# Kernel tuning notes

Hardware: AMD Instinct MI355X
Metric: run time of the kernel (lower is better)

The kernel has to match this reference:

```python
import jax, jax.numpy as jnp
import numpy as np

B, L, E, H, D, DFF = 2, 2048, 1024, 16, 64, 4096
SCALE = D ** 0.5


def rmsnorm(x):
    # NOTE: original uses mean(x*x)**0.5 with no eps and no learned scale
    rms = jnp.sqrt(jnp.mean(x * x, axis=-1, keepdims=True))
    return x / rms


def alibi_matrix():
    i = jnp.arange(L)
    dists = -jnp.abs(i[None, :] - i[:, None]).astype(jnp.float32)  # [L, L]
    slopes = 2.0 ** (-jnp.linspace(1.0, 8.0, H))                   # [H]
    alibi = slopes[:, None, None] * dists                          # [H, L, L]
    causal = jnp.tril(jnp.ones((L, L), dtype=bool))
    return jnp.where(causal[None], alibi, -jnp.inf)[None]          # [1, H, L, L]


def setup_inputs() -> dict:
    key = jax.random.key(0)
    ks = jax.random.split(key, 16)
    s = 0.02
    return {
        "X": jax.random.normal(ks[0], (B, L, E), jnp.float32),
        "encoder_out": jax.random.normal(ks[1], (B, L, E), jnp.float32),
        # self-attention params
        "Wqkv": jax.random.normal(ks[2], (E, 3 * H * D), jnp.float32) * s,
        "bqkv": jnp.zeros((3 * H * D,), jnp.float32),
        "Wo_sa": jax.random.normal(ks[3], (H * D, E), jnp.float32) * s,
        "bo_sa": jnp.zeros((E,), jnp.float32),
        # cross-attention params (computed by torch module but its forward returns X, so unused)
        "Wq": jax.random.normal(ks[4], (E, H * D), jnp.float32) * s,
        "bq": jnp.zeros((H * D,), jnp.float32),
        "Wkv": jax.random.normal(ks[5], (E, 2 * H * D), jnp.float32) * s,
        "bkv": jnp.zeros((2 * H * D,), jnp.float32),
        "Wo_ca": jax.random.normal(ks[6], (H * D, E), jnp.float32) * s,
        "bo_ca": jnp.zeros((E,), jnp.float32),
        # GLU FFN params (bias=False)
        "Ww": jax.random.normal(ks[7], (E, DFF), jnp.float32) * s,
        "Wv": jax.random.normal(ks[8], (E, DFF), jnp.float32) * s,
        "Wout": jax.random.normal(ks[9], (DFF, E), jnp.float32) * s,
    }


def reference(X, encoder_out, Wqkv, bqkv, Wo_sa, bo_sa, Wq, bq, Wkv, bkv,
              Wo_ca, bo_ca, Ww, Wv, Wout):
    alibi = alibi_matrix()

    # ---- self-attention (pre-norm + residual) ----
    h = rmsnorm(X)
    qkv = (h @ Wqkv + bqkv).reshape(B, L, H, 3, D)
    Q, K, V = qkv[..., 0, :], qkv[..., 1, :], qkv[..., 2, :]      # [B, L, H, D]
    scores = jnp.einsum('blhd,bmhd->bhlm', Q, K) / SCALE + alibi  # [B, H, L, L]
    attn = jax.nn.softmax(scores, axis=-1)
    ctx = jnp.einsum('bhlm,bmhd->blhd', attn, V).reshape(B, L, H * D)
    X = X + ctx @ Wo_sa + bo_sa

    # ---- cross-attention stage ----
    # Faithful to source: CrossAttention.forward returns its input X (the
    # normalized tensor) rather than the attention output, so this block is
    # X + rmsnorm(X). Cross-attn params never affect the output.
    X = X + rmsnorm(X)

    # ---- GLU FFN (pre-norm + residual), exact (erf) GELU as in torch F.gelu ----
    h = rmsnorm(X)
    ff = jax.nn.gelu(h @ Ww, approximate=False) * (h @ Wv)
    X = X + ff @ Wout
    return X
```

## Files before the change

### kernel.cpp

```cpp
#include <hip/hip_runtime.h>

#define B_SZ 2
#define L_SEQ 2048
#define E_DIM 1024
#define NH 16
#define DH 64
#define DFF_DIM 4096
#define ROWS (B_SZ * L_SEQ)
#define NCID 80

typedef __attribute__((ext_vector_type(8))) short short8;
typedef __attribute__((ext_vector_type(4))) float f32x4;

__device__ __forceinline__ short f2bf(float f) {
  unsigned u = __builtin_bit_cast(unsigned, f);
  u = (u + 0x7FFFu + ((u >> 16) & 1u)) >> 16;
  return (short)u;
}
__device__ __forceinline__ float bf2f(short s) {
  unsigned u = ((unsigned)(unsigned short)s) << 16;
  return __builtin_bit_cast(float, u);
}

__device__ __forceinline__ void async_copy16(const void* g, void* l) {
  __builtin_amdgcn_global_load_lds(
      (const __attribute__((address_space(1))) void*)g,
      (__attribute__((address_space(3))) void*)l, 16, 0, 0);
}

__device__ __forceinline__ float block_sum256(float v) {
  __shared__ float sbuf[4];
#pragma unroll
  for (int off = 32; off > 0; off >>= 1) v += __shfl_xor(v, off, 64);
  int lane = threadIdx.x & 63, w = threadIdx.x >> 6;
  if (lane == 0) sbuf[w] = v;
  __syncthreads();
  return sbuf[0] + sbuf[1] + sbuf[2] + sbuf[3];
}

__global__ __launch_bounds__(256) void prep_all(
    const float* __restrict__ Wqkv, const float* __restrict__ Wo,
    const float* __restrict__ Ww, const float* __restrict__ Wv,
    const float* __restrict__ Wout, const float* __restrict__ X,
    short* __restrict__ WqkT, short* __restrict__ Wv3T,
    short* __restrict__ WoT, short* __restrict__ Bcat,
    short* __restrict__ WoutT, short* __restrict__ H) {
  __shared__ float tile[32][33];
  int b = blockIdx.x;
  if (b < 16384) {
    const float* W;
    int K, N, mode, bx, by;
    short* Wt;
    if (b < 3072) {
      W = Wqkv; Wt = nullptr; K = 1024; N = 3072; mode = 0;
      bx = b % 96; by = b / 96;
    } else if (b < 4096) {
      int c = b - 3072;
      W = Wo; Wt = WoT; K = 1024; N = 1024; mode = 1;
      bx = c & 31; by = c >> 5;
    } else if (b < 8192) {
      int c = b - 4096;
      W = Ww; Wt = Bcat; K = 1024; N = 4096; mode = 2;
      bx = c & 127; by = c >> 7;
    } else if (b < 12288) {
      int c = b - 8192;
      W = Wv; Wt = Bcat; K = 1024; N = 4096; mode = 3;
      bx = c & 127; by = c >> 7;
    } else {
      int c = b - 12288;
      W = Wout; Wt = WoutT; K = 4096; N = 1024; mode = 1;
      bx = c & 31; by = c >> 5;
    }
    int n0 = bx * 32, k0 = by * 32;
    int tx = threadIdx.x & 31, ty = threadIdx.x >> 5;
#pragma unroll
    for (int i = 0; i < 4; i++)
      tile[ty + 8 * i][tx] = W[(size_t)(k0 + ty + 8 * i) * N + n0 + tx];
    __syncthreads();
#pragma unroll
    for (int i = 0; i < 4; i++) {
      int n = n0 + ty + 8 * i;
      short val = f2bf(tile[tx][ty + 8 * i]);
      if (mode == 0) {
        int h = n / 192, rem = n - h * 192;
        if (rem < 128)
          WqkT[(size_t)(h * 128 + rem) * 1024 + k0 + tx] = val;
        else
          Wv3T[(size_t)(h * 64 + rem - 128) * 1024 + k0 + tx] = val;
      } else {
        int orow = (mode == 1) ? n
                               : ((n >> 6) * 128 + (n & 63) + (mode == 3 ? 64 : 0));
        Wt[(size_t)orow * K + k0 + tx] = val;
      }
    }
  } else {
    size_t row = b - 16384;
    float4 v = ((const float4*)(X + row * E_DIM))[threadIdx.x];
    float ss = v.x * v.x + v.y * v.y + v.z * v.z + v.w * v.w;
    ss = block_sum256(ss);
    float inv = rsqrtf(ss * (1.0f / E_DIM));
    short* h = H + row * E_DIM + (size_t)threadIdx.x * 4;
    h[0] = f2bf(v.x * inv);
    h[1] = f2bf(v.y * inv);
    h[2] = f2bf(v.z * inv);
    h[3] = f2bf(v.w * inv);
  }
}

__global__ __launch_bounds__(256) void resid_rms_fused(
    const float* __restrict__ X, const float* __restrict__ P0,
    const float* __restrict__ P1, const float* __restrict__ bias,
    float* __restrict__ Xout, short* __restrict__ H) {
  size_t row = blockIdx.x;
  int t = threadIdx.x;
  float4 v = ((const float4*)(X + row * E_DIM))[t];
  float4 a = ((const float4*)(P0 + row * E_DIM))[t];
  float4 b = ((const float4*)(P1 + row * E_DIM))[t];
  float4 c = ((const float4*)bias)[t];
  v.x += a.x + b.x + c.x;
  v.y += a.y + b.y + c.y;
  v.z += a.z + b.z + c.z;
  v.w += a.w + b.w + c.w;
  float ss = v.x * v.x + v.y * v.y + v.z * v.z + v.w * v.w;
  ss = block_sum256(ss);
  float inv = rsqrtf(ss * (1.0f / E_DIM));
  float4 o;
  o.x = v.x * (1.0f + inv);
  o.y = v.y * (1.0f + inv);
  o.z = v.z * (1.0f + inv);
  o.w = v.w * (1.0f + inv);
  ((float4*)(Xout + row * E_DIM))[t] = o;
  short* h = H + row * E_DIM + (size_t)t * 4;
  h[0] = f2bf(v.x * inv);
  h[1] = f2bf(v.y * inv);
  h[2] = f2bf(v.z * inv);
  h[3] = f2bf(v.w * inv);
}

__global__ __launch_bounds__(256, 2) void gemm_bt(
    const short* __restrict__ A, const short* __restrict__ Bt,
    const float* __restrict__ bias, void* __restrict__ out,
    void* __restrict__ out2, int M, int N, int K, int epi, int ksplit) {
  __shared__ short smem[128 * 32 * 4];
  short* As0 = smem;
  short* Bs0 = smem + 4096;
  short* As1 = smem + 8192;
  short* Bs1 = smem + 12288;
  int t = threadIdx.x;
  int lane = t & 63;
  int quad = lane >> 4, l16 = lane & 15;
  int wave = t >> 6;
  int wr = wave >> 1, wc = wave & 1;
  int m0 = blockIdx.y * 128, n0 = blockIdx.x * 128;
  int klen = K / ksplit;
  int kstart = blockIdx.z * klen;

  f32x4 acc[4][4];
#pragma unroll
  for (int i = 0; i < 4; i++)
#pragma unroll
    for (int j = 0; j < 4; j++) acc[i][j] = (f32x4){0.f, 0.f, 0.f, 0.f};

  for (int k0 = kstart; k0 < kstart + klen; k0 += 64) {
    __syncthreads();
#pragma unroll
    for (int p = 0; p < 2; p++) {
      int s = p * 256 + t;
      int mm = s >> 2, kk = (s & 3) * 8;
      const short* ag = A + (size_t)(m0 + mm) * K + k0 + kk;
      const short* bg = Bt + (size_t)(n0 + mm) * K + k0 + kk;
      async_copy16(ag, As0 + (size_t)s * 8);
      async_copy16(bg, Bs0 + (size_t)s * 8);
      async_copy16(ag + 32, As1 + (size_t)s * 8);
      async_copy16(bg + 32, Bs1 + (size_t)s * 8);
    }
    __syncthreads();
#pragma unroll
    for (int half = 0; half < 2; half++) {
      const short* As = half ? As1 : As0;
      const short* Bs = half ? Bs1 : Bs0;
      short8 af[4], bfv[4];
#pragma unroll
      for (int i = 0; i < 4; i++) {
        af[i] = *(const short8*)&As[(wr * 64 + i * 16 + l16) * 32 + quad * 8];
        bfv[i] = *(const short8*)&Bs[(wc * 64 + i * 16 + l16) * 32 + quad * 8];
      }
#pragma unroll
      for (int mi = 0; mi < 4; mi++)
#pragma unroll
        for (int ni = 0; ni < 4; ni++)
          acc[mi][ni] = __builtin_amdgcn_mfma_f32_16x16x32_bf16(
              af[mi], bfv[ni], acc[mi][ni], 0, 0, 0);
    }
  }

  if (epi == 5) {
    __syncthreads();
    short* xbuf = smem;
    if (wc == 0) {
#pragma unroll
      for (int mi = 0; mi < 4; mi++)
#pragma unroll
        for (int ni = 0; ni < 4; ni++)
#pragma unroll
          for (int r = 0; r < 4; r++) {
            int rowl = wr * 64 + mi * 16 + quad * 4 + r;
            float v = acc[mi][ni][r];
            float g = 0.5f * v * (1.0f + erff(v * 0.70710678118654752f));
            xbuf[rowl * 68 + ni * 16 + l16] = f2bf(g);
          }
    }
    __syncthreads();
    if (wc == 1) {
      short* FF = (short*)out;
#pragma unroll
      for (int mi = 0; mi < 4; mi++)
#pragma unroll
        for (int ni = 0; ni < 4; ni++)
#pragma unroll
          for (int r = 0; r < 4; r++) {
            int rowl = wr * 64 + mi * 16 + quad * 4 + r;
            int coll = ni * 16 + l16;
            float w = bf2f(xbuf[rowl * 68 + coll]);
            FF[(size_t)(m0 + rowl) * DFF_DIM + blockIdx.x * 64 + coll] =
                f2bf(w * acc[mi][ni][r]);
          }
    }
    return;
  }

#pragma unroll
  for (int mi = 0; mi < 4; mi++) {
#pragma unroll
    for (int ni = 0; ni < 4; ni++) {
      int col = n0 + wc * 64 + ni * 16 + l16;
#pragma unroll
      for (int r = 0; r < 4; r++) {
        int row = m0 + wr * 64 + mi * 16 + quad * 4 + r;
        float v = acc[mi][ni][r];
        if (epi == 4) {
          float* po = (float*)out + (size_t)blockIdx.z * ((size_t)M * N);
          po[(size_t)row * N + col] = v;
        } else if (epi == 6) {
          v += bias[(col >> 7) * 192 + (col & 127)];
          int h = col >> 7, d = col & 63;
          short* dst = ((col >> 6) & 1) ? (short*)out2 : (short*)out;
          int bb = row >> 11, l = row & 2047;
          dst[((size_t)(bb * NH + h) * L_SEQ + l) * DH + d] = f2bf(v);
        } else if (epi == 7) {
          v += bias[(row >> 6) * 192 + 128 + (row & 63)];
          int bb = col >> 11, l = col & 2047;
          ((short*)out)[((size_t)(bb * NH + (row >> 6)) * DH + (row & 63)) *
                            L_SEQ +
                        l] = f2bf(v);
        } else {
          unsafeAtomicAdd((float*)out + (size_t)row * N + col, v);
        }
      }
    }
  }
}

__global__ __launch_bounds__(256) void attn_k(const short* __restrict__ Qh,
                                              const short* __restrict__ Kh,
                                              const short* __restrict__ VTh,
                                              float* __restrict__ OP,
                                              float* __restrict__ RS) {
  int cid = blockIdx.x;
  int bh = blockIdx.y;
  int b = bh >> 4, h = bh & 15;
  int qt, ch;
  if (cid < 8) {
    qt = cid; ch = 0;
  } else if (cid < 24) {
    qt = 8 + ((cid - 8) >> 1); ch = (cid - 8) & 1;
  } else if (cid < 48) {
    qt = 16 + (cid - 24) / 3; ch = (cid - 24) % 3;
  } else {
    qt = 24 + ((cid - 48) >> 2); ch = (cid - 48) & 3;
  }
  int t0 = ch * 8;
  int tend = min(t0 + 8, qt + 1);

  int t = threadIdx.x;
  int wave = t >> 6, lane = t & 63;
  int quad = lane >> 4, l16 = lane & 15;

  __shared__ short kt[64 * 72];
  __shared__ short vt[64 * 72];
  __shared__ short pb[4 * 16 * 70];

  const float slope = exp2f(-(1.0f + (7.0f / 15.0f) * (float)h));
  int iw = qt * 64 + wave * 16;

  short8 qf[2];
  {
    const short* qp = Qh + ((size_t)bh * L_SEQ + iw + l16) * DH + quad * 8;
    qf[0] = *(const short8*)(qp);
    qf[1] = *(const short8*)(qp + 32);
  }

  f32x4 o[4];
#pragma unroll
  for (int i = 0; i < 4; i++) o[i] = (f32x4){0.f, 0.f, 0.f, 0.f};
  float rs[4] = {0.f, 0.f, 0.f, 0.f};
  float crow[4];
  int irow[4];
#pragma unroll
  for (int r = 0; r < 4; r++) {
    irow[r] = iw + quad * 4 + r;
    crow[r] = -slope * (float)irow[r] - 8.0f;
  }

  int sr = t >> 3, sc = (t & 7) * 8;
  const short* kg = Kh + (size_t)bh * L_SEQ * DH;
  const short* vg = VTh + (size_t)bh * DH * L_SEQ;
  short8 kreg[2], vreg[2];
  auto loadKV = [&](int j0) {
    kreg[0] = *(const short8*)(kg + (size_t)(j0 + sr) * DH + sc);
    kreg[1] = *(const short8*)(kg + (size_t)(j0 + sr + 32) * DH + sc);
    vreg[0] = *(const short8*)(vg + (size_t)sr * L_SEQ + j0 + sc);
    vreg[1] = *(const short8*)(vg + (size_t)(sr + 32) * L_SEQ + j0 + sc);
  };
  loadKV(t0 * 64);

  short* pw = &pb[wave * 16 * 70];
  for (int tix = t0; tix < tend; ++tix) {
    int j0 = tix * 64;
    __syncthreads();
    *(short8*)&kt[sr * 72 + sc] = kreg[0];
    *(short8*)&kt[(sr + 32) * 72 + sc] = kreg[1];
    *(short8*)&vt[sr * 72 + sc] = vreg[0];
    *(short8*)&vt[(sr + 32) * 72 + sc] = vreg[1];
    __syncthreads();
    if (tix + 1 < tend) loadKV(j0 + 64);

    f32x4 s[4];
#pragma unroll
    for (int nt = 0; nt < 4; nt++) {
      f32x4 a = (f32x4){0.f, 0.f, 0.f, 0.f};
#pragma unroll
      for (int ks = 0; ks < 2; ks++) {
        short8 bf =
            *(const short8*)&kt[(nt * 16 + l16) * 72 + ks * 32 + quad * 8];
        a = __builtin_amdgcn_mfma_f32_16x16x32_bf16(qf[ks], bf, a, 0, 0, 0);
      }
      s[nt] = a;
    }
    bool diag = (tix == qt);
#pragma unroll
    for (int nt = 0; nt < 4; nt++) {
      int j = j0 + nt * 16 + l16;
      float jb = slope * (float)j;
#pragma unroll
      for (int r = 0; r < 4; r++) {
        float v = __builtin_fmaf(s[nt][r], 0.125f, jb + crow[r]);
        if (diag && j > irow[r]) v = -1e30f;
        float p = __expf(v);
        rs[r] += p;
        pw[(quad * 4 + r) * 70 + nt * 16 + l16] = f2bf(p);
      }
    }
    short8 pf[2];
    pf[0] = *(const short8*)&pw[l16 * 70 + quad * 8];
    pf[1] = *(const short8*)&pw[l16 * 70 + 32 + quad * 8];
#pragma unroll
    for (int nt = 0; nt < 4; nt++) {
#pragma unroll
      for (int ks = 0; ks < 2; ks++) {
        short8 bv =
            *(const short8*)&vt[(nt * 16 + l16) * 72 + ks * 32 + quad * 8];
        o[nt] = __builtin_amdgcn_mfma_f32_16x16x32_bf16(pf[ks], bv, o[nt], 0,
                                                        0, 0);
      }
    }
  }
  float* op = OP + ((size_t)bh * NCID + cid) * 64 * 64;
  float* rsp = RS + ((size_t)bh * NCID + cid) * 64;
#pragma unroll
  for (int r = 0; r < 4; r++) {
#pragma unroll
    for (int off = 1; off < 16; off <<= 1) rs[r] += __shfl_xor(rs[r], off, 64);
    int rowl = wave * 16 + quad * 4 + r;
#pragma unroll
    for (int nt = 0; nt < 4; nt++) op[rowl * 64 + nt * 16 + l16] = o[nt][r];
    if (l16 == 0) rsp[rowl] = rs[r];
  }
}

__global__ __launch_bounds__(256) void attn_merge(const float* __restrict__ OP,
                                                  const float* __restrict__ RS,
                                                  short* __restrict__ ctx) {
  int row = blockIdx.x;
  int b = row >> 11, i = row & 2047;
  int qt = i >> 6, rowin = i & 63;
  int base, nch;
  if (qt < 8) {
    base = qt; nch = 1;
  } else if (qt < 16) {
    base = 8 + 2 * (qt - 8); nch = 2;
  } else if (qt < 24) {
    base = 24 + 3 * (qt - 16); nch = 3;
  } else {
    base = 48 + 4 * (qt - 24); nch = 4;
  }
  int t = threadIdx.x;
  int col = t * 4;
  int h = col >> 6;
  int bh = b * NH + h;
  float4 o = {0.f, 0.f, 0.f, 0.f};
  float l = 0.f;
  for (int s = 0; s < nch; s++) {
    size_t cb = ((size_t)bh * NCID + base + s) * 64 + rowin;
    float4 v = *(const float4*)&OP[cb * 64 + (col & 63)];
    o.x += v.x;
    o.y += v.y;
    o.z += v.z;
    o.w += v.w;
    l += RS[cb];
  }
  float inv = 1.0f / l;
  short* dst = ctx + (size_t)row * (NH * DH) + col;
  dst[0] = f2bf(o.x * inv);
  dst[1] = f2bf(o.y * inv);
  dst[2] = f2bf(o.z * inv);
  dst[3] = f2bf(o.w * inv);
}

extern "C" void kernel_launch(void* const* d_in, const int* in_sizes, int n_in,
                              void* d_out, int out_size, void* d_ws,
                              size_t ws_size, hipStream_t stream) {
  const float* X = (const float*)d_in[0];
  const float* Wqkv = (const float*)d_in[2];
  const float* bqkv = (const float*)d_in[3];
  const float* Wo_sa = (const float*)d_in[4];
  const float* bo_sa = (const float*)d_in[5];
  const float* Ww = (const float*)d_in[12];
  const float* Wv = (const float*)d_in[13];
  const float* Wout = (const float*)d_in[14];

  char* ws = (char*)d_ws;
  auto take = [&](size_t bytes) {
    char* p = ws;
    ws += (bytes + 255) & ~(size_t)255;
    return p;
  };
  short* WqkT = (short*)take((size_t)2048 * 1024 * 2);
  short* Wv3T = (short*)take((size_t)1024 * 1024 * 2);
  short* WoT = (short*)take((size_t)E_DIM * E_DIM * 2);
  short* Bcat = (short*)take((size_t)2 * DFF_DIM * E_DIM * 2);
  short* WoutT = (short*)take((size_t)E_DIM * DFF_DIM * 2);
  short* Hbuf = (short*)take((size_t)ROWS * E_DIM * 2);
  short* Qh = (short*)take((size_t)ROWS * NH * DH * 2);
  short* CTX = (short*)take((size_t)ROWS * NH * DH * 2);
  short* KVb = (short*)take((size_t)2 * B_SZ * NH * L_SEQ * DH * 2);
  char* big = take((size_t)48 * 1024 * 1024);
  short* Kh = KVb;
  short* VTh = KVb + (size_t)B_SZ * NH * L_SEQ * DH;
  float* OP = (float*)big;
  float* RS = OP + (size_t)B_SZ * NH * NCID * 64 * 64;
  short* FF = (short*)(big + (size_t)16 * 1024 * 1024);
  float* Pwo = (float*)FF;
  (void)ws_size;
  (void)in_sizes;
  (void)n_in;
  (void)out_size;

  dim3 blk(256);
  prep_all<<<16384 + ROWS, blk, 0, stream>>>(Wqkv, Wo_sa, Ww, Wv, Wout, X,
                                             WqkT, Wv3T, WoT, Bcat, WoutT,
                                             Hbuf);
  gemm_bt<<<dim3(2048 / 128, ROWS / 128), blk, 0, stream>>>(
      Hbuf, WqkT, bqkv, Qh, Kh, ROWS, 2048, 1024, 6, 1);
  gemm_bt<<<dim3(ROWS / 128, 1024 / 128), blk, 0, stream>>>(
      Wv3T, Hbuf, bqkv, VTh, nullptr, 1024, ROWS, 1024, 7, 1);
  attn_k<<<dim3(NCID, B_SZ * NH), blk, 0, stream>>>(Qh, Kh, VTh, OP, RS);
  attn_merge<<<ROWS, blk, 0, stream>>>(OP, RS, CTX);
  gemm_bt<<<dim3(1024 / 128, ROWS / 128, 2), blk, 0, stream>>>(
      CTX, WoT, nullptr, Pwo, nullptr, ROWS, 1024, 1024, 4, 2);
  resid_rms_fused<<<ROWS, blk, 0, stream>>>(
      X, Pwo, Pwo + (size_t)ROWS * E_DIM, bo_sa, (float*)d_out, Hbuf);
  gemm_bt<<<dim3(2 * DFF_DIM / 128, ROWS / 128), blk, 0, stream>>>(
      Hbuf, Bcat, nullptr, FF, nullptr, ROWS, 2 * DFF_DIM, 1024, 5, 1);
  gemm_bt<<<dim3(1024 / 128, ROWS / 128, 2), blk, 0, stream>>>(
      FF, WoutT, nullptr, d_out, nullptr, ROWS, 1024, 4096, 8, 2);
}
```

Measured before the change: 455.0 us.

## Fuse QKV GEMMs, add V transpose kernel, polynomial GELU, split-K via buffers

Merges the separate QK and transposed-V projections into one 3072-wide GEMM that writes Q, K and V head-major, then adds a small LDS transpose kernel to produce V^T for attention. The GLU epilogue is restructured so each wave pairs gate and value columns held in its own registers (interleaved at 32 columns), which removes the LDS round-trip and the two barriers. Exact erff is replaced by an Abramowitz-Stegun polynomial with rcp and exp, which trades a small accuracy loss for cheaper epilogue arithmetic. The final split-K GEMM now writes partials to scratch instead of using atomics, and a separate add kernel combines them into the output, adding one extra pass over memory.

```diff
diff --git a/kernel.cpp b/kernel.cpp
--- a/kernel.cpp
+++ b/kernel.cpp
@@ -22,6 +22,24 @@
   return __builtin_bit_cast(float, u);
 }
 
+__device__ __forceinline__ float fast_gelu(float x) {
+  float ax = fabsf(x) * 0.70710678118654752f;
+  float t = __builtin_amdgcn_rcpf(__builtin_fmaf(0.3275911f, ax, 1.0f));
+  float p = t * __builtin_fmaf(
+                    t,
+                    __builtin_fmaf(
+                        t,
+                        __builtin_fmaf(t,
+                                       __builtin_fmaf(t, 1.061405429f,
+                                                      -1.453152027f),
+                                       1.421413741f),
+                        -0.284496736f),
+                    0.254829592f);
+  float erf = 1.0f - p * __expf(-ax * ax);
+  erf = copysignf(erf, x);
+  return 0.5f * x * (1.0f + erf);
+}
+
 __device__ __forceinline__ void async_copy16(const void* g, void* l) {
   __builtin_amdgcn_global_load_lds(
       (const __attribute__((address_space(1))) void*)g,
@@ -42,17 +60,17 @@
     const float* __restrict__ Wqkv, const float* __restrict__ Wo,
     const float* __restrict__ Ww, const float* __restrict__ Wv,
     const float* __restrict__ Wout, const float* __restrict__ X,
-    short* __restrict__ WqkT, short* __restrict__ Wv3T,
-    short* __restrict__ WoT, short* __restrict__ Bcat,
-    short* __restrict__ WoutT, short* __restrict__ H) {
+    short* __restrict__ Bqkv3, short* __restrict__ WoT,
+    short* __restrict__ Bcat, short* __restrict__ WoutT,
+    short* __restrict__ H) {
   __shared__ float tile[32][33];
   int b = blockIdx.x;
   if (b < 16384) {
     const float* W;
+    short* Wt;
     int K, N, mode, bx, by;
-    short* Wt;
     if (b < 3072) {
-      W = Wqkv; Wt = nullptr; K = 1024; N = 3072; mode = 0;
+      W = Wqkv; Wt = Bqkv3; K = 1024; N = 3072; mode = 1;
       bx = b % 96; by = b / 96;
     } else if (b < 4096) {
       int c = b - 3072;
@@ -80,18 +98,10 @@
 #pragma unroll
     for (int i = 0; i < 4; i++) {
       int n = n0 + ty + 8 * i;
-      short val = f2bf(tile[tx][ty + 8 * i]);
-      if (mode == 0) {
-        int h = n / 192, rem = n - h * 192;
-        if (rem < 128)
-          WqkT[(size_t)(h * 128 + rem) * 1024 + k0 + tx] = val;
-        else
-          Wv3T[(size_t)(h * 64 + rem - 128) * 1024 + k0 + tx] = val;
-      } else {
-        int orow = (mode == 1) ? n
-                               : ((n >> 6) * 128 + (n & 63) + (mode == 3 ? 64 : 0));
-        Wt[(size_t)orow * K + k0 + tx] = val;
-      }
+      int orow = (mode == 1)
+                     ? n
+                     : ((n >> 5) * 64 + (n & 31) + (mode == 3 ? 32 : 0));
+      Wt[(size_t)orow * K + k0 + tx] = f2bf(tile[tx][ty + 8 * i]);
     }
   } else {
     size_t row = b - 16384;
@@ -137,10 +147,25 @@
   h[3] = f2bf(v.w * inv);
 }
 
+__global__ __launch_bounds__(256) void add2_k(const float* __restrict__ P0,
+                                              const float* __restrict__ P1,
+                                              float* __restrict__ out) {
+  size_t i = (size_t)blockIdx.x * 256 + threadIdx.x;
+  float4 v = ((const float4*)out)[i];
+  float4 a = ((const float4*)P0)[i];
+  float4 b = ((const float4*)P1)[i];
+  v.x += a.x + b.x;
+  v.y += a.y + b.y;
+  v.z += a.z + b.z;
+  v.w += a.w + b.w;
+  ((float4*)out)[i] = v;
+}
+
 __global__ __launch_bounds__(256, 2) void gemm_bt(
     const short* __restrict__ A, const short* __restrict__ Bt,
     const float* __restrict__ bias, void* __restrict__ out,
-    void* __restrict__ out2, int M, int N, int K, int epi, int ksplit) {
+    void* __restrict__ out2, void* __restrict__ out3, int M, int N, int K,
+    int epi, int ksplit) {
   __shared__ short smem[128 * 32 * 4];
   short* As0 = smem;
   short* Bs0 = smem + 4096;
@@ -195,37 +220,19 @@
   }
 
   if (epi == 5) {
-    __syncthreads();
-    short* xbuf = smem;
-    if (wc == 0) {
-#pragma unroll
-      for (int mi = 0; mi < 4; mi++)
-#pragma unroll
-        for (int ni = 0; ni < 4; ni++)
-#pragma unroll
-          for (int r = 0; r < 4; r++) {
-            int rowl = wr * 64 + mi * 16 + quad * 4 + r;
-            float v = acc[mi][ni][r];
-            float g = 0.5f * v * (1.0f + erff(v * 0.70710678118654752f));
-            xbuf[rowl * 68 + ni * 16 + l16] = f2bf(g);
-          }
-    }
-    __syncthreads();
-    if (wc == 1) {
-      short* FF = (short*)out;
-#pragma unroll
-      for (int mi = 0; mi < 4; mi++)
-#pragma unroll
-        for (int ni = 0; ni < 4; ni++)
-#pragma unroll
-          for (int r = 0; r < 4; r++) {
-            int rowl = wr * 64 + mi * 16 + quad * 4 + r;
-            int coll = ni * 16 + l16;
-            float w = bf2f(xbuf[rowl * 68 + coll]);
-            FF[(size_t)(m0 + rowl) * DFF_DIM + blockIdx.x * 64 + coll] =
-                f2bf(w * acc[mi][ni][r]);
-          }
-    }
+    short* FF = (short*)out;
+    int ffbase = blockIdx.x * 64 + wc * 32;
+#pragma unroll
+    for (int mi = 0; mi < 4; mi++)
+#pragma unroll
+      for (int ni = 0; ni < 2; ni++)
+#pragma unroll
+        for (int r = 0; r < 4; r++) {
+          int rowl = wr * 64 + mi * 16 + quad * 4 + r;
+          float g = fast_gelu(acc[mi][ni][r]);
+          FF[(size_t)(m0 + rowl) * DFF_DIM + ffbase + ni * 16 + l16] =
+              f2bf(g * acc[mi][ni + 2][r]);
+        }
     return;
   }
 
@@ -241,23 +248,42 @@
         if (epi == 4) {
           float* po = (float*)out + (size_t)blockIdx.z * ((size_t)M * N);
           po[(size_t)row * N + col] = v;
-        } else if (epi == 6) {
-          v += bias[(col >> 7) * 192 + (col & 127)];
-          int h = col >> 7, d = col & 63;
-          short* dst = ((col >> 6) & 1) ? (short*)out2 : (short*)out;
+        } else {
+          v += bias[col];
+          int h = col / 192;
+          int rem = col - h * 192;
+          int ty = rem >> 6, d = rem & 63;
+          short* dst = (ty == 0) ? (short*)out
+                                 : ((ty == 1) ? (short*)out2 : (short*)out3);
           int bb = row >> 11, l = row & 2047;
           dst[((size_t)(bb * NH + h) * L_SEQ + l) * DH + d] = f2bf(v);
-        } else if (epi == 7) {
-          v += bias[(row >> 6) * 192 + 128 + (row & 63)];
-          int bb = col >> 11, l = col & 2047;
-          ((short*)out)[((size_t)(bb * NH + (row >> 6)) * DH + (row & 63)) *
-                            L_SEQ +
-                        l] = f2bf(v);
-        } else {
-          unsafeAtomicAdd((float*)out + (size_t)row * N + col, v);
         }
       }
     }
+  }
+}
+
+__global__ __launch_bounds__(256) void v_transp(const short* __restrict__ Vh,
+                                                short* __restrict__ VTh) {
+  int lt = blockIdx.x, bh = blockIdx.y;
+  __shared__ short vtile[64 * 72];
+  int t = threadIdx.x;
+  int r = t >> 3, c = (t & 7) * 8;
+  const short* src = Vh + ((size_t)bh * L_SEQ + lt * 64) * DH;
+#pragma unroll
+  for (int p = 0; p < 2; p++) {
+    int row = r + p * 32;
+    short8 vv = *(const short8*)(src + (size_t)row * DH + c);
+    *(short8*)&vtile[row * 72 + c] = vv;
+  }
+  __syncthreads();
+#pragma unroll
+  for (int p = 0; p < 2; p++) {
+    int d = r + p * 32;
+    short8 o;
+#pragma unroll
+    for (int u = 0; u < 8; u++) o[u] = vtile[(c + u) * 72 + d];
+    *(short8*)(VTh + ((size_t)bh * DH + d) * L_SEQ + lt * 64 + c) = o;
   }
 }
 
@@ -445,22 +471,22 @@
     ws += (bytes + 255) & ~(size_t)255;
     return p;
   };
-  short* WqkT = (short*)take((size_t)2048 * 1024 * 2);
-  short* Wv3T = (short*)take((size_t)1024 * 1024 * 2);
+  short* Bqkv3 = (short*)take((size_t)3072 * 1024 * 2);
   short* WoT = (short*)take((size_t)E_DIM * E_DIM * 2);
   short* Bcat = (short*)take((size_t)2 * DFF_DIM * E_DIM * 2);
   short* WoutT = (short*)take((size_t)E_DIM * DFF_DIM * 2);
   short* Hbuf = (short*)take((size_t)ROWS * E_DIM * 2);
   short* Qh = (short*)take((size_t)ROWS * NH * DH * 2);
+  short* Kh = (short*)take((size_t)ROWS * NH * DH * 2);
+  short* Vh = (short*)take((size_t)ROWS * NH * DH * 2);
+  short* VTh = (short*)take((size_t)ROWS * NH * DH * 2);
   short* CTX = (short*)take((size_t)ROWS * NH * DH * 2);
-  short* KVb = (short*)take((size_t)2 * B_SZ * NH * L_SEQ * DH * 2);
   char* big = take((size_t)48 * 1024 * 1024);
-  short* Kh = KVb;
-  short* VTh = KVb + (size_t)B_SZ * NH * L_SEQ * DH;
   float* OP = (float*)big;
   float* RS = OP + (size_t)B_SZ * NH * NCID * 64 * 64;
-  short* FF = (short*)(big + (size_t)16 * 1024 * 1024);
-  float* Pwo = (float*)FF;
+  float* Pwo = (float*)(big + (size_t)16 * 1024 * 1024);
+  short* FF = (short*)Pwo;
+  float* Pwout = (float*)Qh;
   (void)ws_size;
   (void)in_sizes;
   (void)n_in;
@@ -468,20 +494,21 @@
 
   dim3 blk(256);
   prep_all<<<16384 + ROWS, blk, 0, stream>>>(Wqkv, Wo_sa, Ww, Wv, Wout, X,
-                                             WqkT, Wv3T, WoT, Bcat, WoutT,
-                                             Hbuf);
-  gemm_bt<<<dim3(2048 / 128, ROWS / 128), blk, 0, stream>>>(
-      Hbuf, WqkT, bqkv, Qh, Kh, ROWS, 2048, 1024, 6, 1);
-  gemm_bt<<<dim3(ROWS / 128, 1024 / 128), blk, 0, stream>>>(
-      Wv3T, Hbuf, bqkv, VTh, nullptr, 1024, ROWS, 1024, 7, 1);
+                                             Bqkv3, WoT, Bcat, WoutT, Hbuf);
+  gemm_bt<<<dim3(3072 / 128, ROWS / 128), blk, 0, stream>>>(
+      Hbuf, Bqkv3, bqkv, Qh, Kh, Vh, ROWS, 3072, 1024, 6, 1);
+  v_transp<<<dim3(L_SEQ / 64, B_SZ * NH), blk, 0, stream>>>(Vh, VTh);
   attn_k<<<dim3(NCID, B_SZ * NH), blk, 0, stream>>>(Qh, Kh, VTh, OP, RS);
   attn_merge<<<ROWS, blk, 0, stream>>>(OP, RS, CTX);
   gemm_bt<<<dim3(1024 / 128, ROWS / 128, 2), blk, 0, stream>>>(
-      CTX, WoT, nullptr, Pwo, nullptr, ROWS, 1024, 1024, 4, 2);
+      CTX, WoT, nullptr, Pwo, nullptr, nullptr, ROWS, 1024, 1024, 4, 2);
   resid_rms_fused<<<ROWS, blk, 0, stream>>>(
       X, Pwo, Pwo + (size_t)ROWS * E_DIM, bo_sa, (float*)d_out, Hbuf);
   gemm_bt<<<dim3(2 * DFF_DIM / 128, ROWS / 128), blk, 0, stream>>>(
-      Hbuf, Bcat, nullptr, FF, nullptr, ROWS, 2 * DFF_DIM, 1024, 5, 1);
+      Hbuf, Bcat, nullptr, FF, nullptr, nullptr, ROWS, 2 * DFF_DIM, 1024, 5,
+      1);
   gemm_bt<<<dim3(1024 / 128, ROWS / 128, 2), blk, 0, stream>>>(
-      FF, WoutT, nullptr, d_out, nullptr, ROWS, 1024, 4096, 8, 2);
-}
+      FF, WoutT, nullptr, Pwout, nullptr, nullptr, ROWS, 1024, 4096, 4, 2);
+  add2_k<<<ROWS * E_DIM / (256 * 4), blk, 0, stream>>>(
+      Pwout, Pwout + (size_t)ROWS * E_DIM, (float*)d_out);
+}
```

Result: faster. 422.7 us (-7.1%).
